# Kernel optimization log

Hardware: AMD Instinct MI355X
Metric: run time of the kernel (lower is better)

Reference implementation:

```python
import jax, jax.numpy as jnp
import numpy as np

B, C, H, W = 16, 256, 32, 32
AD, SC, R = 16, 32, 4


def _conv1x1(x, w, b):
    # x: [B,Cin,H,W], w: [Cout,Cin], b: [Cout]
    return jnp.einsum('oc,bchw->bohw', w, x) + b[None, :, None, None]


def setup_inputs() -> dict:
    key = jax.random.key(0)
    ks = jax.random.split(key, 12)
    p = lambda k, shape: (jax.random.normal(k, shape, dtype=jnp.float32) * 0.02)
    return {
        'x': jax.random.normal(ks[0], (B, C, H, W), dtype=jnp.float32),
        'fc1_w': p(ks[1], (C // R, C)), 'fc1_b': jnp.zeros((C // R,), jnp.float32),
        'fc2_w': p(ks[2], (C, C // R)), 'fc2_b': jnp.zeros((C,), jnp.float32),
        'qkv_w': p(ks[3], (AD * 2 + SC, SC)), 'qkv_b': jnp.zeros((AD * 2 + SC,), jnp.float32),
        'proj_w': p(ks[4], (SC, SC)), 'proj_b': jnp.zeros((SC,), jnp.float32),
        'ffn1_w': p(ks[5], (4 * C, C)), 'ffn1_b': jnp.zeros((4 * C,), jnp.float32),
        'ffn2_w': p(ks[6], (C, 4 * C)), 'ffn2_b': jnp.zeros((C,), jnp.float32),
    }


def reference(x, fc1_w, fc1_b, fc2_w, fc2_b, qkv_w, qkv_b, proj_w, proj_b,
              ffn1_w, ffn1_b, ffn2_w, ffn2_b):
    # --- DynamicChannelSelect: SE gate then channel split ---
    s = x.mean(axis=(2, 3), keepdims=True)                       # [B,C,1,1]
    s = jax.nn.relu(_conv1x1(s, fc1_w, fc1_b))
    s = jax.nn.sigmoid(_conv1x1(s, fc2_w, fc2_b))
    xg = x * s
    attn_part, non_attn_part = xg[:, :SC], xg[:, SC:]

    # --- SHSA: single-head self-attention on SC channels ---
    qkv = _conv1x1(attn_part, qkv_w, qkv_b)                      # [B,2*AD+SC,H,W]
    q = qkv[:, :AD].reshape(B, AD, H * W)
    k = qkv[:, AD:2 * AD].reshape(B, AD, H * W)
    v = qkv[:, 2 * AD:].reshape(B, SC, H * W)
    scale = AD ** -0.5
    attn = jax.nn.softmax(jnp.einsum('bcn,bcm->bnm', q, k) * scale, axis=-1)  # [B,N,N]
    out = jnp.einsum('bcm,bnm->bcn', v, attn).reshape(B, SC, H, W)
    attn_out = _conv1x1(out, proj_w, proj_b)

    # --- concat + 1x1-conv FFN ---
    y = jnp.concatenate([attn_out, non_attn_part], axis=1)       # [B,C,H,W]
    h = jax.nn.relu(_conv1x1(y, ffn1_w, ffn1_b))                 # [B,4C,H,W]
    return _conv1x1(h, ffn2_w, ffn2_b)                           # [B,C,H,W]
```

## Files before the change

kernel.cpp:

```cpp
#include <hip/hip_runtime.h>
#include <cstdint>
#include <cstddef>

#define BB 16
#define CC 256
#define NP 1024

typedef __attribute__((ext_vector_type(8))) short bf16x8;
typedef __attribute__((ext_vector_type(4))) float f32x4;
typedef unsigned short u16;

__device__ __forceinline__ u16 f2bf(float f) {
    union { float f; uint32_t u; } v; v.f = f;
    uint32_t u = v.u;
    return (u16)((u + 0x7FFFu + ((u >> 16) & 1u)) >> 16);
}

__global__ __launch_bounds__(256)
void se_mean_conv_kernel(const float* __restrict__ x, float* __restrict__ s_mean,
                         const float* __restrict__ w1, u16* __restrict__ d1,
                         const float* __restrict__ w2, u16* __restrict__ d2) {
    int blk = blockIdx.x;
    int t = threadIdx.x;
    if (blk < BB * CC) {
        const float* p = x + (size_t)blk * NP;
        float4 v = *(const float4*)(p + t * 4);
        float s = (v.x + v.y) + (v.z + v.w);
#pragma unroll
        for (int off = 32; off; off >>= 1) s += __shfl_down(s, off, 64);
        __shared__ float red[4];
        if ((t & 63) == 0) red[t >> 6] = s;
        __syncthreads();
        if (t == 0) s_mean[blk] = (red[0] + red[1] + red[2] + red[3]) * (1.0f / NP);
    } else {
        int blk2 = blk - BB * CC;
        const float* src = (blk2 < 256) ? w1 : w2;
        u16* dst = (blk2 < 256) ? d1 : d2;
        int i = ((blk2 & 255) * 256 + t) * 4;
        float4 v = *(const float4*)(src + i);
        ushort4 o;
        o.x = f2bf(v.x); o.y = f2bf(v.y); o.z = f2bf(v.z); o.w = f2bf(v.w);
        *(ushort4*)(dst + i) = o;
    }
}

__global__ __launch_bounds__(256)
void se_mlp_kernel(const float* __restrict__ s_mean,
                   const float* __restrict__ fc1_w, const float* __restrict__ fc1_b,
                   const float* __restrict__ fc2_w, const float* __restrict__ fc2_b,
                   float* __restrict__ sig) {
    int b = blockIdx.x;
    __shared__ float sm[CC];
    __shared__ float h1[64];
    int t = threadIdx.x;
    sm[t] = s_mean[b * CC + t];
    __syncthreads();
    if (t < 64) {
        float a = fc1_b[t];
        for (int c = 0; c < CC; ++c) a += fc1_w[t * CC + c] * sm[c];
        h1[t] = fmaxf(a, 0.f);
    }
    __syncthreads();
    float a = fc2_b[t];
#pragma unroll 8
    for (int c = 0; c < 64; ++c) a += fc2_w[t * 64 + c] * h1[c];
    sig[b * CC + t] = 1.f / (1.f + __expf(-a));
}

__global__ __launch_bounds__(256)
void scale_transpose_qkv_kernel(const float* __restrict__ x, const float* __restrict__ sig,
                                const float* __restrict__ qW, const float* __restrict__ qB,
                                u16* __restrict__ ygt, u16* __restrict__ Qt,
                                u16* __restrict__ Kt, u16* __restrict__ Vb) {
    int nt = blockIdx.x, ct = blockIdx.y, b = blockIdx.z;
    __shared__ float tile[64][65];
    __shared__ float ws[64 * 32];
    __shared__ float bs[64];
    __shared__ float vtile[32][64];
    int t = threadIdx.x;
    const float* Xb = x + ((size_t)b * CC + ct * 64) * NP + nt * 64;
    if (ct == 0) {
        for (int e = t; e < 2048; e += 256) ws[e] = qW[e];
        if (t < 64) bs[t] = qB[t];
    }
#pragma unroll
    for (int p = 0; p < 4; ++p) {
        int e = t + p * 256;
        int c = e >> 4, n4 = (e & 15) * 4;
        float4 v = *(const float4*)&Xb[(size_t)c * NP + n4];
        float sc = sig[b * CC + ct * 64 + c];
        v.x *= sc; v.y *= sc; v.z *= sc; v.w *= sc;
        tile[c][n4] = v.x; tile[c][n4 + 1] = v.y; tile[c][n4 + 2] = v.z; tile[c][n4 + 3] = v.w;
    }
    __syncthreads();
    u16* Yb = ygt + ((size_t)b * NP + nt * 64) * CC + ct * 64;
#pragma unroll
    for (int p = 0; p < 4; ++p) {
        int e = t + p * 256;
        int n = e >> 4, c4 = (e & 15) * 4;
        if (ct * 64 + c4 >= 32) {
            ushort4 o;
            o.x = f2bf(tile[c4][n]);     o.y = f2bf(tile[c4 + 1][n]);
            o.z = f2bf(tile[c4 + 2][n]); o.w = f2bf(tile[c4 + 3][n]);
            *(ushort4*)&Yb[(size_t)n * CC + c4] = o;
        }
    }
    if (ct == 0) {
        int nn = t & 63, g = t >> 6;
        int n = nt * 64 + nn;
        float acc[16];
#pragma unroll
        for (int oc = 0; oc < 16; ++oc) {
            int o = g * 16 + oc;
            float a = bs[o];
#pragma unroll
            for (int c = 0; c < 32; ++c) a += ws[o * 32 + c] * tile[c][nn];
            acc[oc] = a;
        }
        if (g == 0) {
            u16* qr = Qt + ((size_t)b * NP + n) * 32;
            ushort4 z4; z4.x = 0; z4.y = 0; z4.z = 0; z4.w = 0;
#pragma unroll
            for (int j = 0; j < 16; j += 4) {
                ushort4 o4;
                o4.x = f2bf(acc[j] * 0.25f);     o4.y = f2bf(acc[j + 1] * 0.25f);
                o4.z = f2bf(acc[j + 2] * 0.25f); o4.w = f2bf(acc[j + 3] * 0.25f);
                *(ushort4*)&qr[j] = o4;
            }
            *(ushort4*)&qr[16] = z4; *(ushort4*)&qr[20] = z4;
            *(ushort4*)&qr[24] = z4; *(ushort4*)&qr[28] = z4;
        } else if (g == 1) {
            u16* kr = Kt + ((size_t)b * NP + n) * 32;
            ushort4 z4; z4.x = 0; z4.y = 0; z4.z = 0; z4.w = 0;
#pragma unroll
            for (int j = 0; j < 16; j += 4) {
                ushort4 k4;
                k4.x = f2bf(acc[j]);     k4.y = f2bf(acc[j + 1]);
                k4.z = f2bf(acc[j + 2]); k4.w = f2bf(acc[j + 3]);
                *(ushort4*)&kr[j] = k4;
            }
            *(ushort4*)&kr[16] = z4; *(ushort4*)&kr[20] = z4;
            *(ushort4*)&kr[24] = z4; *(ushort4*)&kr[28] = z4;
        } else {
#pragma unroll
            for (int oc = 0; oc < 16; ++oc) vtile[(g - 2) * 16 + oc][nn] = acc[oc];
        }
        __syncthreads();
        for (int e = t; e < 2048; e += 256) {
            int c = e >> 6, nn2 = e & 63;
            Vb[(size_t)b * 32 * NP + (size_t)c * NP + nt * 64 + nn2] = f2bf(vtile[c][nn2]);
        }
    }
}

__global__ __launch_bounds__(256)
void attn_mfma_kernel(const u16* __restrict__ Qt, const u16* __restrict__ Kt,
                      const u16* __restrict__ Vb,
                      const float* __restrict__ proj_w, const float* __restrict__ proj_b,
                      u16* __restrict__ ygt) {
    int b = blockIdx.x >> 6;
    int n0 = (blockIdx.x & 63) * 16;
    __shared__ __align__(16) u16 P_lds[4][16][40];
    __shared__ float al_lds[4][16];
    __shared__ float sm_lds[4][16];
    __shared__ float sl_lds[4][16];
    __shared__ float O_lds[4][16][33];
    __shared__ float pw_s[32][32];
    __shared__ float pb_s[32];
    int t = threadIdx.x;
    int w = t >> 6, lane = t & 63;
    int q = lane >> 4, idx = lane & 15;

    for (int e = t; e < 1024; e += 256) pw_s[e >> 5][e & 31] = proj_w[e];
    if (t < 32) pb_s[t] = proj_b[t];
    __syncthreads();

    const u16* Qb = Qt + (size_t)b * NP * 32;
    const u16* Kb = Kt + (size_t)b * NP * 32;
    const u16* Vp = Vb + (size_t)b * 32 * NP;

    int nrow = n0 + idx;
    bf16x8 aq = *(const bf16x8*)&Qb[(size_t)nrow * 32 + q * 8];

    f32x4 O0 = {0.f, 0.f, 0.f, 0.f}, O1 = {0.f, 0.f, 0.f, 0.f};
    float m_run[4] = {-1e30f, -1e30f, -1e30f, -1e30f};
    float l_run[4] = {0.f, 0.f, 0.f, 0.f};

    int mbase = w * 256;
    for (int m0 = mbase; m0 < mbase + 256; m0 += 32) {
        bf16x8 bk0 = *(const bf16x8*)&Kb[(size_t)(m0 + idx) * 32 + q * 8];
        bf16x8 bk1 = *(const bf16x8*)&Kb[(size_t)(m0 + 16 + idx) * 32 + q * 8];
        bf16x8 va0 = *(const bf16x8*)&Vp[(size_t)idx * NP + m0 + q * 8];
        bf16x8 va1 = *(const bf16x8*)&Vp[(size_t)(16 + idx) * NP + m0 + q * 8];
        f32x4 z = {0.f, 0.f, 0.f, 0.f};
        f32x4 S0 = __builtin_amdgcn_mfma_f32_16x16x32_bf16(aq, bk0, z, 0, 0, 0);
        f32x4 S1 = __builtin_amdgcn_mfma_f32_16x16x32_bf16(aq, bk1, z, 0, 0, 0);
        float mx[4], p0[4], p1[4], alpha[4];
#pragma unroll
        for (int r = 0; r < 4; ++r) mx[r] = fmaxf(S0[r], S1[r]);
#pragma unroll
        for (int off = 1; off < 16; off <<= 1)
#pragma unroll
            for (int r = 0; r < 4; ++r) mx[r] = fmaxf(mx[r], __shfl_xor(mx[r], off, 64));
#pragma unroll
        for (int r = 0; r < 4; ++r) {
            float nm = fmaxf(m_run[r], mx[r]);
            alpha[r] = __expf(m_run[r] - nm);
            m_run[r] = nm;
            p0[r] = __expf(S0[r] - nm);
            p1[r] = __expf(S1[r] - nm);
        }
#pragma unroll
        for (int r = 0; r < 4; ++r) {
            float s = p0[r] + p1[r];
#pragma unroll
            for (int off = 1; off < 16; off <<= 1) s += __shfl_xor(s, off, 64);
            l_run[r] = l_run[r] * alpha[r] + s;
        }
#pragma unroll
        for (int r = 0; r < 4; ++r) {
            P_lds[w][q * 4 + r][idx]      = f2bf(p0[r]);
            P_lds[w][q * 4 + r][idx + 16] = f2bf(p1[r]);
        }
        if (idx == 0) {
#pragma unroll
            for (int r = 0; r < 4; ++r) al_lds[w][q * 4 + r] = alpha[r];
        }
        float an = al_lds[w][idx];
#pragma unroll
        for (int r = 0; r < 4; ++r) { O0[r] *= an; O1[r] *= an; }
        bf16x8 pf = *(const bf16x8*)&P_lds[w][idx][q * 8];
        O0 = __builtin_amdgcn_mfma_f32_16x16x32_bf16(va0, pf, O0, 0, 0, 0);
        O1 = __builtin_amdgcn_mfma_f32_16x16x32_bf16(va1, pf, O1, 0, 0, 0);
    }
    if (idx == 0) {
#pragma unroll
        for (int r = 0; r < 4; ++r) {
            sm_lds[w][q * 4 + r] = m_run[r];
            sl_lds[w][q * 4 + r] = l_run[r];
        }
    }
#pragma unroll
    for (int r = 0; r < 4; ++r) {
        O_lds[w][idx][q * 4 + r]      = O0[r];
        O_lds[w][idx][q * 4 + r + 16] = O1[r];
    }
    __syncthreads();
    if (w == 0) {
        float m0_ = sm_lds[0][idx], m1 = sm_lds[1][idx], m2 = sm_lds[2][idx], m3 = sm_lds[3][idx];
        float gm = fmaxf(fmaxf(m0_, m1), fmaxf(m2, m3));
        float e0 = __expf(m0_ - gm), e1 = __expf(m1 - gm);
        float e2 = __expf(m2 - gm), e3 = __expf(m3 - gm);
        float linv = 1.f / (sl_lds[0][idx] * e0 + sl_lds[1][idx] * e1 +
                            sl_lds[2][idx] * e2 + sl_lds[3][idx] * e3);
#pragma unroll
        for (int r = 0; r < 4; ++r) {
            int c0 = q * 4 + r;
            O_lds[0][idx][c0] = (O_lds[0][idx][c0] * e0 + O_lds[1][idx][c0] * e1 +
                                 O_lds[2][idx][c0] * e2 + O_lds[3][idx][c0] * e3) * linv;
            int c1 = c0 + 16;
            O_lds[0][idx][c1] = (O_lds[0][idx][c1] * e0 + O_lds[1][idx][c1] * e1 +
                                 O_lds[2][idx][c1] * e2 + O_lds[3][idx][c1] * e3) * linv;
        }
        float o0[4], o1[4];
#pragma unroll
        for (int r = 0; r < 4; ++r) { o0[r] = pb_s[q * 4 + r]; o1[r] = pb_s[q * 4 + r + 16]; }
#pragma unroll
        for (int c = 0; c < 32; ++c) {
            float xv = O_lds[0][idx][c];
#pragma unroll
            for (int r = 0; r < 4; ++r) {
                o0[r] += pw_s[q * 4 + r][c] * xv;
                o1[r] += pw_s[q * 4 + r + 16][c] * xv;
            }
        }
        u16* yrow = ygt + ((size_t)b * NP + n0 + idx) * CC;
        ushort4 w0, w1;
        w0.x = f2bf(o0[0]); w0.y = f2bf(o0[1]); w0.z = f2bf(o0[2]); w0.w = f2bf(o0[3]);
        w1.x = f2bf(o1[0]); w1.y = f2bf(o1[1]); w1.z = f2bf(o1[2]); w1.w = f2bf(o1[3]);
        *(ushort4*)&yrow[q * 4] = w0;
        *(ushort4*)&yrow[q * 4 + 16] = w1;
    }
}

template <int K, bool RELU>
__global__ __launch_bounds__(256)
void mfma_gemm_kernel(const u16* __restrict__ A, const u16* __restrict__ Bt,
                      const float* __restrict__ bias, u16* __restrict__ Y, int M) {
    __shared__ __align__(16) u16 As[2][128][64];
    __shared__ __align__(16) u16 Bs[2][128][64];
    constexpr int NIT = K / 64;
    int mt = blockIdx.x, nt = blockIdx.y;
    const u16* Ab = A + (size_t)mt * 128 * K;
    const u16* Bb = Bt + (size_t)nt * 128 * K;
    int t = threadIdx.x;
    int w = t >> 6, lane = t & 63;
    int q = lane >> 4, idx = lane & 15;
    int wr = (w >> 1) * 64, wc = (w & 1) * 64;
    int srow = lane >> 3;
    int gch = (lane & 7) ^ srow;

    f32x4 acc[4][4];
#pragma unroll
    for (int i = 0; i < 4; ++i)
#pragma unroll
        for (int j = 0; j < 4; ++j) { f32x4 z = {0.f, 0.f, 0.f, 0.f}; acc[i][j] = z; }

#define ISSUE_LOADS(buf, k0)                                                              \
    {                                                                                     \
        _Pragma("unroll")                                                                 \
        for (int p = 0; p < 4; ++p) {                                                     \
            int r = w * 32 + p * 8 + srow;                                                \
            __builtin_amdgcn_global_load_lds(                                             \
                (const __attribute__((address_space(1))) void*)(Ab + (size_t)r * K + (k0) + gch * 8), \
                (__attribute__((address_space(3))) void*)(&As[buf][w * 32 + p * 8][0]),   \
                16, 0, 0);                                                                \
        }                                                                                 \
        _Pragma("unroll")                                                                 \
        for (int p = 0; p < 4; ++p) {                                                     \
            int r = w * 32 + p * 8 + srow;                                                \
            __builtin_amdgcn_global_load_lds(                                             \
                (const __attribute__((address_space(1))) void*)(Bb + (size_t)r * K + (k0) + gch * 8), \
                (__attribute__((address_space(3))) void*)(&Bs[buf][w * 32 + p * 8][0]),   \
                16, 0, 0);                                                                \
        }                                                                                 \
    }

    ISSUE_LOADS(0, 0)
    for (int ki = 0; ki < NIT; ++ki) {
        int cur = ki & 1;
        __syncthreads();
        if (ki + 1 < NIT) ISSUE_LOADS(cur ^ 1, (ki + 1) * 64)
#pragma unroll
        for (int h = 0; h < 2; ++h) {
            bf16x8 af[4], bfr[4];
#pragma unroll
            for (int i = 0; i < 4; ++i)
                af[i] = *(const bf16x8*)&As[cur][wr + i * 16 + idx][(((q + 4 * h) ^ (idx & 7)) * 8)];
#pragma unroll
            for (int j = 0; j < 4; ++j)
                bfr[j] = *(const bf16x8*)&Bs[cur][wc + j * 16 + idx][(((q + 4 * h) ^ (idx & 7)) * 8)];
#pragma unroll
            for (int i = 0; i < 4; ++i)
#pragma unroll
                for (int j = 0; j < 4; ++j)
                    acc[i][j] = __builtin_amdgcn_mfma_f32_16x16x32_bf16(af[i], bfr[j], acc[i][j], 0, 0, 0);
        }
    }
#undef ISSUE_LOADS

#pragma unroll
    for (int i = 0; i < 4; ++i) {
        int m0 = mt * 128 + wr + i * 16 + q * 4;
        float b0 = bias[m0], b1 = bias[m0 + 1], b2 = bias[m0 + 2], b3 = bias[m0 + 3];
#pragma unroll
        for (int j = 0; j < 4; ++j) {
            int n = nt * 128 + wc + j * 16 + idx;
            f32x4 v = acc[i][j];
            float r0 = v.x + b0, r1 = v.y + b1, r2 = v.z + b2, r3 = v.w + b3;
            if (RELU) {
                r0 = fmaxf(r0, 0.f); r1 = fmaxf(r1, 0.f);
                r2 = fmaxf(r2, 0.f); r3 = fmaxf(r3, 0.f);
            }
            ushort4 o;
            o.x = f2bf(r0); o.y = f2bf(r1); o.z = f2bf(r2); o.w = f2bf(r3);
            *(ushort4*)&Y[(size_t)n * (size_t)M + m0] = o;
        }
    }
}

template <int K>
__global__ __launch_bounds__(256)
void mfma_gemm_n64_kernel(const u16* __restrict__ A, const u16* __restrict__ Bt,
                          const float* __restrict__ bias, float* __restrict__ Y, int M) {
    __shared__ __align__(16) u16 As[2][128][64];
    __shared__ __align__(16) u16 Bs[2][64][64];
    constexpr int NIT = K / 64;
    int mt = blockIdx.x, nt = blockIdx.y;
    const u16* Ab = A + (size_t)mt * 128 * K;
    const u16* Bb = Bt + (size_t)nt * 64 * K;
    int t = threadIdx.x;
    int w = t >> 6, lane = t & 63;
    int q = lane >> 4, idx = lane & 15;
    int wr = (w >> 1) * 64, wc = (w & 1) * 32;
    int srow = lane >> 3;
    int gch = (lane & 7) ^ srow;

    f32x4 acc[4][2];
#pragma unroll
    for (int i = 0; i < 4; ++i)
#pragma unroll
        for (int j = 0; j < 2; ++j) { f32x4 z = {0.f, 0.f, 0.f, 0.f}; acc[i][j] = z; }

#define ISSUE_LOADS64(buf, k0)                                                            \
    {                                                                                     \
        _Pragma("unroll")                                                                 \
        for (int p = 0; p < 4; ++p) {                                                     \
            int r = w * 32 + p * 8 + srow;                                                \
            __builtin_amdgcn_global_load_lds(                                             \
                (const __attribute__((address_space(1))) void*)(Ab + (size_t)r * K + (k0) + gch * 8), \
                (__attribute__((address_space(3))) void*)(&As[buf][w * 32 + p * 8][0]),   \
                16, 0, 0);                                                                \
        }                                                                                 \
        _Pragma("unroll")                                                                 \
        for (int p = 0; p < 2; ++p) {                                                     \
            int r = w * 16 + p * 8 + srow;                                                \
            __builtin_amdgcn_global_load_lds(                                             \
                (const __attribute__((address_space(1))) void*)(Bb + (size_t)r * K + (k0) + gch * 8), \
                (__attribute__((address_space(3))) void*)(&Bs[buf][w * 16 + p * 8][0]),   \
                16, 0, 0);                                                                \
        }                                                                                 \
    }

    ISSUE_LOADS64(0, 0)
    for (int ki = 0; ki < NIT; ++ki) {
        int cur = ki & 1;
        __syncthreads();
        if (ki + 1 < NIT) ISSUE_LOADS64(cur ^ 1, (ki + 1) * 64)
#pragma unroll
        for (int h = 0; h < 2; ++h) {
            bf16x8 af[4], bfr[2];
#pragma unroll
            for (int i = 0; i < 4; ++i)
                af[i] = *(const bf16x8*)&As[cur][wr + i * 16 + idx][(((q + 4 * h) ^ (idx & 7)) * 8)];
#pragma unroll
            for (int j = 0; j < 2; ++j)
                bfr[j] = *(const bf16x8*)&Bs[cur][wc + j * 16 + idx][(((q + 4 * h) ^ (idx & 7)) * 8)];
#pragma unroll
            for (int i = 0; i < 4; ++i)
#pragma unroll
                for (int j = 0; j < 2; ++j)
                    acc[i][j] = __builtin_amdgcn_mfma_f32_16x16x32_bf16(af[i], bfr[j], acc[i][j], 0, 0, 0);
        }
    }
#undef ISSUE_LOADS64

#pragma unroll
    for (int i = 0; i < 4; ++i) {
        int m0 = mt * 128 + wr + i * 16 + q * 4;
        float b0 = bias[m0], b1 = bias[m0 + 1], b2 = bias[m0 + 2], b3 = bias[m0 + 3];
#pragma unroll
        for (int j = 0; j < 2; ++j) {
            int ng = nt * 64 + wc + j * 16 + idx;
            int bb = ng >> 10, nn = ng & 1023;
            f32x4 v = acc[i][j];
            float* p = Y + ((size_t)bb * M + m0) * NP + nn;
            p[0]      = v.x + b0;
            p[NP]     = v.y + b1;
            p[2 * NP] = v.z + b2;
            p[3 * NP] = v.w + b3;
        }
    }
}

extern "C" void kernel_launch(void* const* d_in, const int* in_sizes, int n_in,
                              void* d_out, int out_size, void* d_ws, size_t ws_size,
                              hipStream_t stream) {
    const float* x      = (const float*)d_in[0];
    const float* fc1_w  = (const float*)d_in[1];
    const float* fc1_b  = (const float*)d_in[2];
    const float* fc2_w  = (const float*)d_in[3];
    const float* fc2_b  = (const float*)d_in[4];
    const float* qkv_w  = (const float*)d_in[5];
    const float* qkv_b  = (const float*)d_in[6];
    const float* proj_w = (const float*)d_in[7];
    const float* proj_b = (const float*)d_in[8];
    const float* ffn1_w = (const float*)d_in[9];
    const float* ffn1_b = (const float*)d_in[10];
    const float* ffn2_w = (const float*)d_in[11];
    const float* ffn2_b = (const float*)d_in[12];
    float* out = (float*)d_out;

    u16* w1b = (u16*)d_ws;
    u16* w2b = w1b + 262144;
    u16* ygt = w2b + 262144;
    u16* ht  = ygt + (size_t)BB * NP * CC;
    float* sig    = (float*)ht;
    float* s_mean = sig + BB * CC;
    u16* Qt = (u16*)(s_mean + BB * CC);
    u16* Kt = Qt + (size_t)BB * NP * 32;
    u16* Vb = Kt + (size_t)BB * NP * 32;

    se_mean_conv_kernel<<<BB * CC + 512, 256, 0, stream>>>(x, s_mean, ffn1_w, w1b, ffn2_w, w2b);
    se_mlp_kernel<<<BB, 256, 0, stream>>>(s_mean, fc1_w, fc1_b, fc2_w, fc2_b, sig);
    scale_transpose_qkv_kernel<<<dim3(16, 4, BB), 256, 0, stream>>>(
        x, sig, qkv_w, qkv_b, ygt, Qt, Kt, Vb);
    attn_mfma_kernel<<<BB * 64, 256, 0, stream>>>(Qt, Kt, Vb, proj_w, proj_b, ygt);

    mfma_gemm_kernel<256, true><<<dim3(8, 128), 256, 0, stream>>>(
        w1b, ygt, ffn1_b, ht, 1024);
    mfma_gemm_n64_kernel<1024><<<dim3(2, 256), 256, 0, stream>>>(
        w2b, ht, ffn2_b, out, 256);
}
```

Before: 180.1 us.

## Fuse FFN GEMMs into one kernel and fold SE MLP into scale kernel

Replaces the two separate FFN GEMM kernels with a single kernel that keeps each 64-pixel tile's hidden activations in LDS. It streams W1 and W2 tiles through a double buffer, avoiding the global write and read of the 4C hidden tensor. The SE MLP kernel is removed: each block of the scale/transpose kernel recomputes the gate for its channels. The trade-off is lower occupancy, one block per CU, small MFMA tiles and redundant fc1 computation in every block.

Measured after the change: 201.6 us. +12.0%, slower.

```diff
diff --git a/kernel.cpp b/kernel.cpp
--- a/kernel.cpp
+++ b/kernel.cpp
@@ -45,30 +45,9 @@
 }
 
 __global__ __launch_bounds__(256)
-void se_mlp_kernel(const float* __restrict__ s_mean,
-                   const float* __restrict__ fc1_w, const float* __restrict__ fc1_b,
-                   const float* __restrict__ fc2_w, const float* __restrict__ fc2_b,
-                   float* __restrict__ sig) {
-    int b = blockIdx.x;
-    __shared__ float sm[CC];
-    __shared__ float h1[64];
-    int t = threadIdx.x;
-    sm[t] = s_mean[b * CC + t];
-    __syncthreads();
-    if (t < 64) {
-        float a = fc1_b[t];
-        for (int c = 0; c < CC; ++c) a += fc1_w[t * CC + c] * sm[c];
-        h1[t] = fmaxf(a, 0.f);
-    }
-    __syncthreads();
-    float a = fc2_b[t];
-#pragma unroll 8
-    for (int c = 0; c < 64; ++c) a += fc2_w[t * 64 + c] * h1[c];
-    sig[b * CC + t] = 1.f / (1.f + __expf(-a));
-}
-
-__global__ __launch_bounds__(256)
-void scale_transpose_qkv_kernel(const float* __restrict__ x, const float* __restrict__ sig,
+void scale_transpose_qkv_kernel(const float* __restrict__ x, const float* __restrict__ s_mean,
+                                const float* __restrict__ fc1_w, const float* __restrict__ fc1_b,
+                                const float* __restrict__ fc2_w, const float* __restrict__ fc2_b,
                                 const float* __restrict__ qW, const float* __restrict__ qB,
                                 u16* __restrict__ ygt, u16* __restrict__ Qt,
                                 u16* __restrict__ Kt, u16* __restrict__ Vb) {
@@ -77,8 +56,12 @@
     __shared__ float ws[64 * 32];
     __shared__ float bs[64];
     __shared__ float vtile[32][64];
+    __shared__ float smean_s[CC];
+    __shared__ float h1[64];
+    __shared__ float sig_l[64];
     int t = threadIdx.x;
     const float* Xb = x + ((size_t)b * CC + ct * 64) * NP + nt * 64;
+    smean_s[t] = s_mean[b * CC + t];
     if (ct == 0) {
         for (int e = t; e < 2048; e += 256) ws[e] = qW[e];
         if (t < 64) bs[t] = qB[t];
@@ -88,9 +71,22 @@
         int e = t + p * 256;
         int c = e >> 4, n4 = (e & 15) * 4;
         float4 v = *(const float4*)&Xb[(size_t)c * NP + n4];
-        float sc = sig[b * CC + ct * 64 + c];
-        v.x *= sc; v.y *= sc; v.z *= sc; v.w *= sc;
         tile[c][n4] = v.x; tile[c][n4 + 1] = v.y; tile[c][n4 + 2] = v.z; tile[c][n4 + 3] = v.w;
+    }
+    __syncthreads();
+    if (t < 64) {
+        float a = fc1_b[t];
+#pragma unroll 4
+        for (int c = 0; c < CC; ++c) a += fc1_w[t * CC + c] * smean_s[c];
+        h1[t] = fmaxf(a, 0.f);
+    }
+    __syncthreads();
+    if (t < 64) {
+        int c = ct * 64 + t;
+        float a = fc2_b[c];
+#pragma unroll 8
+        for (int j = 0; j < 64; ++j) a += fc2_w[c * 64 + j] * h1[j];
+        sig_l[t] = 1.f / (1.f + __expf(-a));
     }
     __syncthreads();
     u16* Yb = ygt + ((size_t)b * NP + nt * 64) * CC + ct * 64;
@@ -100,21 +96,26 @@
         int n = e >> 4, c4 = (e & 15) * 4;
         if (ct * 64 + c4 >= 32) {
             ushort4 o;
-            o.x = f2bf(tile[c4][n]);     o.y = f2bf(tile[c4 + 1][n]);
-            o.z = f2bf(tile[c4 + 2][n]); o.w = f2bf(tile[c4 + 3][n]);
+            o.x = f2bf(tile[c4][n] * sig_l[c4]);
+            o.y = f2bf(tile[c4 + 1][n] * sig_l[c4 + 1]);
+            o.z = f2bf(tile[c4 + 2][n] * sig_l[c4 + 2]);
+            o.w = f2bf(tile[c4 + 3][n] * sig_l[c4 + 3]);
             *(ushort4*)&Yb[(size_t)n * CC + c4] = o;
         }
     }
     if (ct == 0) {
         int nn = t & 63, g = t >> 6;
         int n = nt * 64 + nn;
+        float xs[32];
+#pragma unroll
+        for (int c = 0; c < 32; ++c) xs[c] = tile[c][nn] * sig_l[c];
         float acc[16];
 #pragma unroll
         for (int oc = 0; oc < 16; ++oc) {
             int o = g * 16 + oc;
             float a = bs[o];
 #pragma unroll
-            for (int c = 0; c < 32; ++c) a += ws[o * 32 + c] * tile[c][nn];
+            for (int c = 0; c < 32; ++c) a += ws[o * 32 + c] * xs[c];
             acc[oc] = a;
         }
         if (g == 0) {
@@ -283,173 +284,124 @@
     }
 }
 
-template <int K, bool RELU>
+#define STAGE_W1(R0, DST)                                                                   \
+    {                                                                                       \
+        _Pragma("unroll")                                                                   \
+        for (int is_ = 0; is_ < 4; ++is_) {                                                 \
+            int seg_ = is_ * 4 + w;                                                         \
+            int chunk_ = seg_ * 64 + lane;                                                  \
+            int row_ = chunk_ >> 5, c_ = chunk_ & 31;                                       \
+            __builtin_amdgcn_global_load_lds(                                               \
+                (const __attribute__((address_space(1))) void*)(w1 + (((size_t)((R0) + row_)) << 8) + ((c_ ^ (row_ & 7)) << 3)), \
+                (__attribute__((address_space(3))) void*)((DST) + seg_ * 512),              \
+                16, 0, 0);                                                                  \
+        }                                                                                   \
+    }
+#define STAGE_W2(C0, KOFF, DST)                                                             \
+    {                                                                                       \
+        _Pragma("unroll")                                                                   \
+        for (int is_ = 0; is_ < 2; ++is_) {                                                 \
+            int seg_ = is_ * 4 + w;                                                         \
+            int chunk_ = seg_ * 64 + lane;                                                  \
+            int row_ = chunk_ >> 4, c_ = chunk_ & 15;                                       \
+            __builtin_amdgcn_global_load_lds(                                               \
+                (const __attribute__((address_space(1))) void*)(w2 + (((size_t)((C0) + row_)) << 10) + (KOFF) + ((c_ ^ (row_ & 7)) << 3)), \
+                (__attribute__((address_space(3))) void*)((DST) + seg_ * 512),              \
+                16, 0, 0);                                                                  \
+        }                                                                                   \
+    }
+
 __global__ __launch_bounds__(256)
-void mfma_gemm_kernel(const u16* __restrict__ A, const u16* __restrict__ Bt,
-                      const float* __restrict__ bias, u16* __restrict__ Y, int M) {
-    __shared__ __align__(16) u16 As[2][128][64];
-    __shared__ __align__(16) u16 Bs[2][128][64];
-    constexpr int NIT = K / 64;
-    int mt = blockIdx.x, nt = blockIdx.y;
-    const u16* Ab = A + (size_t)mt * 128 * K;
-    const u16* Bb = Bt + (size_t)nt * 128 * K;
+void ffn_fused_kernel(const u16* __restrict__ ygt,
+                      const u16* __restrict__ w1,
+                      const float* __restrict__ b1,
+                      const u16* __restrict__ w2,
+                      const float* __restrict__ b2,
+                      float* __restrict__ out) {
+    __shared__ __align__(16) u16 y_lds[64 * 256];
+    __shared__ __align__(16) u16 h_lds[64 * 128];
+    __shared__ __align__(16) u16 wst[2][8192];
+    int nt = blockIdx.x;
     int t = threadIdx.x;
     int w = t >> 6, lane = t & 63;
     int q = lane >> 4, idx = lane & 15;
-    int wr = (w >> 1) * 64, wc = (w & 1) * 64;
-    int srow = lane >> 3;
-    int gch = (lane & 7) ^ srow;
-
-    f32x4 acc[4][4];
-#pragma unroll
-    for (int i = 0; i < 4; ++i)
-#pragma unroll
-        for (int j = 0; j < 4; ++j) { f32x4 z = {0.f, 0.f, 0.f, 0.f}; acc[i][j] = z; }
-
-#define ISSUE_LOADS(buf, k0)                                                              \
-    {                                                                                     \
-        _Pragma("unroll")                                                                 \
-        for (int p = 0; p < 4; ++p) {                                                     \
-            int r = w * 32 + p * 8 + srow;                                                \
-            __builtin_amdgcn_global_load_lds(                                             \
-                (const __attribute__((address_space(1))) void*)(Ab + (size_t)r * K + (k0) + gch * 8), \
-                (__attribute__((address_space(3))) void*)(&As[buf][w * 32 + p * 8][0]),   \
-                16, 0, 0);                                                                \
-        }                                                                                 \
-        _Pragma("unroll")                                                                 \
-        for (int p = 0; p < 4; ++p) {                                                     \
-            int r = w * 32 + p * 8 + srow;                                                \
-            __builtin_amdgcn_global_load_lds(                                             \
-                (const __attribute__((address_space(1))) void*)(Bb + (size_t)r * K + (k0) + gch * 8), \
-                (__attribute__((address_space(3))) void*)(&Bs[buf][w * 32 + p * 8][0]),   \
-                16, 0, 0);                                                                \
-        }                                                                                 \
-    }
-
-    ISSUE_LOADS(0, 0)
-    for (int ki = 0; ki < NIT; ++ki) {
-        int cur = ki & 1;
-        __syncthreads();
-        if (ki + 1 < NIT) ISSUE_LOADS(cur ^ 1, (ki + 1) * 64)
-#pragma unroll
-        for (int h = 0; h < 2; ++h) {
-            bf16x8 af[4], bfr[4];
-#pragma unroll
-            for (int i = 0; i < 4; ++i)
-                af[i] = *(const bf16x8*)&As[cur][wr + i * 16 + idx][(((q + 4 * h) ^ (idx & 7)) * 8)];
-#pragma unroll
-            for (int j = 0; j < 4; ++j)
-                bfr[j] = *(const bf16x8*)&Bs[cur][wc + j * 16 + idx][(((q + 4 * h) ^ (idx & 7)) * 8)];
-#pragma unroll
-            for (int i = 0; i < 4; ++i)
-#pragma unroll
-                for (int j = 0; j < 4; ++j)
-                    acc[i][j] = __builtin_amdgcn_mfma_f32_16x16x32_bf16(af[i], bfr[j], acc[i][j], 0, 0, 0);
-        }
-    }
-#undef ISSUE_LOADS
-
-#pragma unroll
-    for (int i = 0; i < 4; ++i) {
-        int m0 = mt * 128 + wr + i * 16 + q * 4;
-        float b0 = bias[m0], b1 = bias[m0 + 1], b2 = bias[m0 + 2], b3 = bias[m0 + 3];
-#pragma unroll
-        for (int j = 0; j < 4; ++j) {
-            int n = nt * 128 + wc + j * 16 + idx;
-            f32x4 v = acc[i][j];
-            float r0 = v.x + b0, r1 = v.y + b1, r2 = v.z + b2, r3 = v.w + b3;
-            if (RELU) {
-                r0 = fmaxf(r0, 0.f); r1 = fmaxf(r1, 0.f);
-                r2 = fmaxf(r2, 0.f); r3 = fmaxf(r3, 0.f);
+    int sw = idx & 7;
+
+    const u16* ysrc = ygt + (size_t)nt * 64 * 256;
+#pragma unroll
+    for (int is = 0; is < 8; ++is) {
+        int seg = is * 4 + w;
+        int chunk = seg * 64 + lane;
+        int row = chunk >> 5, c = chunk & 31;
+        __builtin_amdgcn_global_load_lds(
+            (const __attribute__((address_space(1))) void*)(ysrc + ((size_t)row << 8) + ((c ^ (row & 7)) << 3)),
+            (__attribute__((address_space(3))) void*)(y_lds + seg * 512),
+            16, 0, 0);
+    }
+    STAGE_W1(0, &wst[0][0])
+    __syncthreads();
+
+    f32x4 acc[16];
+#pragma unroll
+    for (int i = 0; i < 16; ++i) { f32x4 z = {0.f, 0.f, 0.f, 0.f}; acc[i] = z; }
+
+    int buf = 0;
+    for (int hc = 0; hc < 8; ++hc) {
+        for (int s = 0; s < 4; ++s) {
+            if (s < 3) STAGE_W1(hc * 128 + (s + 1) * 32, &wst[buf ^ 1][0])
+            else       STAGE_W2(0, (size_t)hc * 128, &wst[buf ^ 1][0])
+#pragma unroll
+            for (int ti = 0; ti < 2; ++ti) {
+                f32x4 a2 = {0.f, 0.f, 0.f, 0.f};
+#pragma unroll
+                for (int kwin = 0; kwin < 8; ++kwin) {
+                    int ga = kwin * 4 + q;
+                    bf16x8 af = *(const bf16x8*)&wst[buf][((ti * 16 + idx) * 32 + (ga ^ sw)) * 8];
+                    bf16x8 bfr = *(const bf16x8*)&y_lds[((w * 16 + idx) * 32 + (ga ^ sw)) * 8];
+                    a2 = __builtin_amdgcn_mfma_f32_16x16x32_bf16(af, bfr, a2, 0, 0, 0);
+                }
+                int k2g = hc * 128 + s * 32 + ti * 16 + q * 4;
+                float4 bb = *(const float4*)&b1[k2g];
+                float r0 = fmaxf(a2[0] + bb.x, 0.f), r1 = fmaxf(a2[1] + bb.y, 0.f);
+                float r2 = fmaxf(a2[2] + bb.z, 0.f), r3 = fmaxf(a2[3] + bb.w, 0.f);
+                ushort4 o;
+                o.x = f2bf(r0); o.y = f2bf(r1); o.z = f2bf(r2); o.w = f2bf(r3);
+                int g = s * 4 + ti * 2 + (q >> 1);
+                *(ushort4*)&h_lds[(w * 16 + idx) * 128 + (g ^ sw) * 8 + (q & 1) * 4] = o;
             }
-            ushort4 o;
-            o.x = f2bf(r0); o.y = f2bf(r1); o.z = f2bf(r2); o.w = f2bf(r3);
-            *(ushort4*)&Y[(size_t)n * (size_t)M + m0] = o;
-        }
-    }
-}
-
-template <int K>
-__global__ __launch_bounds__(256)
-void mfma_gemm_n64_kernel(const u16* __restrict__ A, const u16* __restrict__ Bt,
-                          const float* __restrict__ bias, float* __restrict__ Y, int M) {
-    __shared__ __align__(16) u16 As[2][128][64];
-    __shared__ __align__(16) u16 Bs[2][64][64];
-    constexpr int NIT = K / 64;
-    int mt = blockIdx.x, nt = blockIdx.y;
-    const u16* Ab = A + (size_t)mt * 128 * K;
-    const u16* Bb = Bt + (size_t)nt * 64 * K;
-    int t = threadIdx.x;
-    int w = t >> 6, lane = t & 63;
-    int q = lane >> 4, idx = lane & 15;
-    int wr = (w >> 1) * 64, wc = (w & 1) * 32;
-    int srow = lane >> 3;
-    int gch = (lane & 7) ^ srow;
-
-    f32x4 acc[4][2];
-#pragma unroll
-    for (int i = 0; i < 4; ++i)
-#pragma unroll
-        for (int j = 0; j < 2; ++j) { f32x4 z = {0.f, 0.f, 0.f, 0.f}; acc[i][j] = z; }
-
-#define ISSUE_LOADS64(buf, k0)                                                            \
-    {                                                                                     \
-        _Pragma("unroll")                                                                 \
-        for (int p = 0; p < 4; ++p) {                                                     \
-            int r = w * 32 + p * 8 + srow;                                                \
-            __builtin_amdgcn_global_load_lds(                                             \
-                (const __attribute__((address_space(1))) void*)(Ab + (size_t)r * K + (k0) + gch * 8), \
-                (__attribute__((address_space(3))) void*)(&As[buf][w * 32 + p * 8][0]),   \
-                16, 0, 0);                                                                \
-        }                                                                                 \
-        _Pragma("unroll")                                                                 \
-        for (int p = 0; p < 2; ++p) {                                                     \
-            int r = w * 16 + p * 8 + srow;                                                \
-            __builtin_amdgcn_global_load_lds(                                             \
-                (const __attribute__((address_space(1))) void*)(Bb + (size_t)r * K + (k0) + gch * 8), \
-                (__attribute__((address_space(3))) void*)(&Bs[buf][w * 16 + p * 8][0]),   \
-                16, 0, 0);                                                                \
-        }                                                                                 \
-    }
-
-    ISSUE_LOADS64(0, 0)
-    for (int ki = 0; ki < NIT; ++ki) {
-        int cur = ki & 1;
-        __syncthreads();
-        if (ki + 1 < NIT) ISSUE_LOADS64(cur ^ 1, (ki + 1) * 64)
-#pragma unroll
-        for (int h = 0; h < 2; ++h) {
-            bf16x8 af[4], bfr[2];
-#pragma unroll
-            for (int i = 0; i < 4; ++i)
-                af[i] = *(const bf16x8*)&As[cur][wr + i * 16 + idx][(((q + 4 * h) ^ (idx & 7)) * 8)];
-#pragma unroll
-            for (int j = 0; j < 2; ++j)
-                bfr[j] = *(const bf16x8*)&Bs[cur][wc + j * 16 + idx][(((q + 4 * h) ^ (idx & 7)) * 8)];
-#pragma unroll
-            for (int i = 0; i < 4; ++i)
-#pragma unroll
-                for (int j = 0; j < 2; ++j)
-                    acc[i][j] = __builtin_amdgcn_mfma_f32_16x16x32_bf16(af[i], bfr[j], acc[i][j], 0, 0, 0);
-        }
-    }
-#undef ISSUE_LOADS64
-
-#pragma unroll
-    for (int i = 0; i < 4; ++i) {
-        int m0 = mt * 128 + wr + i * 16 + q * 4;
-        float b0 = bias[m0], b1 = bias[m0 + 1], b2 = bias[m0 + 2], b3 = bias[m0 + 3];
-#pragma unroll
-        for (int j = 0; j < 2; ++j) {
-            int ng = nt * 64 + wc + j * 16 + idx;
-            int bb = ng >> 10, nn = ng & 1023;
-            f32x4 v = acc[i][j];
-            float* p = Y + ((size_t)bb * M + m0) * NP + nn;
-            p[0]      = v.x + b0;
-            p[NP]     = v.y + b1;
-            p[2 * NP] = v.z + b2;
-            p[3 * NP] = v.w + b3;
-        }
+            __syncthreads();
+            buf ^= 1;
+        }
+        for (int s2 = 0; s2 < 8; ++s2) {
+            if (s2 < 7)      STAGE_W2((s2 + 1) * 32, (size_t)hc * 128, &wst[buf ^ 1][0])
+            else if (hc < 7) STAGE_W1((hc + 1) * 128, &wst[buf ^ 1][0])
+#pragma unroll
+            for (int ti = 0; ti < 2; ++ti) {
+                int ct = s2 * 2 + ti;
+#pragma unroll
+                for (int kwin = 0; kwin < 4; ++kwin) {
+                    int ga = kwin * 4 + q;
+                    bf16x8 af = *(const bf16x8*)&wst[buf][((ti * 16 + idx) * 16 + (ga ^ sw)) * 8];
+                    bf16x8 bfr = *(const bf16x8*)&h_lds[((w * 16 + idx) * 16 + (ga ^ sw)) * 8];
+                    acc[ct] = __builtin_amdgcn_mfma_f32_16x16x32_bf16(af, bfr, acc[ct], 0, 0, 0);
+                }
+            }
+            __syncthreads();
+            buf ^= 1;
+        }
+    }
+
+    int nfl = nt * 64 + w * 16 + idx;
+    int bo = nfl >> 10, npix = nfl & 1023;
+#pragma unroll
+    for (int ct = 0; ct < 16; ++ct) {
+        int c0 = ct * 16 + q * 4;
+        float4 bb = *(const float4*)&b2[c0];
+        float* p = out + ((size_t)bo * 256 + c0) * 1024 + npix;
+        p[0]        = acc[ct][0] + bb.x;
+        p[1024]     = acc[ct][1] + bb.y;
+        p[2 * 1024] = acc[ct][2] + bb.z;
+        p[3 * 1024] = acc[ct][3] + bb.w;
     }
 }
 
@@ -474,21 +426,14 @@
     u16* w1b = (u16*)d_ws;
     u16* w2b = w1b + 262144;
     u16* ygt = w2b + 262144;
-    u16* ht  = ygt + (size_t)BB * NP * CC;
-    float* sig    = (float*)ht;
-    float* s_mean = sig + BB * CC;
+    float* s_mean = (float*)(ygt + (size_t)BB * NP * CC);
     u16* Qt = (u16*)(s_mean + BB * CC);
     u16* Kt = Qt + (size_t)BB * NP * 32;
     u16* Vb = Kt + (size_t)BB * NP * 32;
 
     se_mean_conv_kernel<<<BB * CC + 512, 256, 0, stream>>>(x, s_mean, ffn1_w, w1b, ffn2_w, w2b);
-    se_mlp_kernel<<<BB, 256, 0, stream>>>(s_mean, fc1_w, fc1_b, fc2_w, fc2_b, sig);
     scale_transpose_qkv_kernel<<<dim3(16, 4, BB), 256, 0, stream>>>(
-        x, sig, qkv_w, qkv_b, ygt, Qt, Kt, Vb);
+        x, s_mean, fc1_w, fc1_b, fc2_w, fc2_b, qkv_w, qkv_b, ygt, Qt, Kt, Vb);
     attn_mfma_kernel<<<BB * 64, 256, 0, stream>>>(Qt, Kt, Vb, proj_w, proj_b, ygt);
-
-    mfma_gemm_kernel<256, true><<<dim3(8, 128), 256, 0, stream>>>(
-        w1b, ygt, ffn1_b, ht, 1024);
-    mfma_gemm_n64_kernel<1024><<<dim3(2, 256), 256, 0, stream>>>(
-        w2b, ht, ffn2_b, out, 256);
-}
+    ffn_fused_kernel<<<256, 256, 0, stream>>>(ygt, w1b, ffn1_b, w2b, ffn2_b, out);
+}
```
